# Optimization experiments

Measured on AMD Instinct MI355X. Metric: run time of the kernel, lower is better.

Reference implementation:

```python
import jax, jax.numpy as jnp
import numpy as np

MUL = 128          # multiplicity of each irrep (mul_in == mul_out)
DIMS = (1, 3, 5)   # ir dims for 0e, 1o, 2e
G = 32             # num_indices (weight groups)
N = 2048           # number of elements (rows)
W_FLAT = MUL * MUL * len(DIMS)


def setup_inputs() -> dict:
    key = jax.random.key(0)
    k0, k1, k2, kw = jax.random.split(key, 4)
    x0 = jax.random.normal(k0, (N, MUL, DIMS[0]), jnp.float32)
    x1 = jax.random.normal(k1, (N, MUL, DIMS[1]), jnp.float32)
    x2 = jax.random.normal(k2, (N, MUL, DIMS[2]), jnp.float32)
    w = jax.random.normal(kw, (G, W_FLAT), jnp.float32)
    # variable group sizes summing exactly to N (Repeats(num_index_counts))
    counts = np.random.default_rng(0).multinomial(N, np.ones(G) / G)
    repeats = jnp.asarray(counts, jnp.int32)
    return {"x0": x0, "x1": x1, "x2": x2, "w": w, "repeats": repeats}


def reference(x0, x1, x2, w, repeats):
    # Indexed equivariant linear: row n uses weight group seg[n], where the
    # first repeats[0] rows map to group 0, next repeats[1] rows to group 1, ...
    num_indices = w.shape[0]
    n = x0.shape[0]
    # scale/sqrt(num_indices) from the module times 1/sqrt(mul_in) path norm
    alpha = jnp.float32(1.0 / np.sqrt(num_indices * MUL))
    seg = jnp.searchsorted(jnp.cumsum(repeats), jnp.arange(n), side="right")
    outs = []
    off = 0
    for x in (x0, x1, x2):
        w_ir = w[:, off : off + MUL * MUL].reshape(num_indices, MUL, MUL)
        off += MUL * MUL
        w_el = w_ir[seg]  # (N, mul_in, mul_out) gathered per element
        # x: (N, mul_in, ir_dim) mul_ir layout -> y: (N, mul_out, ir_dim)
        y = jnp.einsum("nmi,nmo->noi", x, w_el) * alpha
        outs.append(y)
    return tuple(outs)
```

## Files before the change

### kernel.cpp

```cpp
#include <hip/hip_runtime.h>


#define NGROUP 32
#define WSTRIDE (128 * 128 * 3)
#define ALPHA 0.015625f

#define CAP0 96
#define CAP01 256
#define GRID_BLOCKS 544

#define LDS_FLOATS 6144

template <int D, int TR, int RP>
__device__ inline void run_ir(int lt, const float* __restrict__ x,
                              const float* __restrict__ w_base_ir,
                              const int* __restrict__ repeats,
                              float* __restrict__ obase,
                              float* __restrict__ Xs) {
  int off = 0, g = -1, row0 = 0, nr = 0;
  int tacc = 0;
  for (int gg = 0; gg < NGROUP; ++gg) {
    int c = repeats[gg];
    int tg = (c + TR - 1) / TR;
    if (lt < tacc + tg) {
      int tig = lt - tacc;
      g = gg;
      row0 = off + tig * TR;
      nr = min(TR, c - tig * TR);
      break;
    }
    tacc += tg;
    off += c;
  }
  if (g < 0) return;

  const int tid = threadIdx.x;
  const int to = tid & 31;
  const int tr = tid >> 5;

  constexpr int ROWELEMS = 128 * D;
  constexpr int BMELEMS = TR * ROWELEMS;

  {
    const float4* xsrc = (const float4*)(x + (size_t)row0 * ROWELEMS);
    float4* xdst = (float4*)Xs;
    const int limit4 = nr * (ROWELEMS / 4);
    constexpr int Q = BMELEMS / 4;
    const float4 z = make_float4(0.f, 0.f, 0.f, 0.f);
    for (int q = tid; q < Q; q += 256) xdst[q] = (q < limit4) ? xsrc[q] : z;
  }
  __syncthreads();

  int xoff[RP];
  int nloc[RP];
  int iofr[RP];
#pragma unroll
  for (int rr = 0; rr < RP; ++rr) {
    int r = tr * RP + rr;
    int nl = r / D;
    int i = r - nl * D;
    nloc[rr] = nl;
    iofr[rr] = i;
    xoff[rr] = nl * ROWELEMS + i;
  }

  const float* w_g = w_base_ir + (size_t)g * WSTRIDE;
  const float4* wp = (const float4*)w_g + to;

  float acc[RP][4];
#pragma unroll
  for (int rr = 0; rr < RP; ++rr)
#pragma unroll
    for (int oj = 0; oj < 4; ++oj) acc[rr][oj] = 0.0f;

#pragma unroll 8
  for (int m = 0; m < 128; ++m) {
    const float4 wf = wp[m * 32];
    float xs[RP];
#pragma unroll
    for (int rr = 0; rr < RP; ++rr) xs[rr] = Xs[xoff[rr] + m * D];
#pragma unroll
    for (int rr = 0; rr < RP; ++rr) {
      acc[rr][0] += xs[rr] * wf.x;
      acc[rr][1] += xs[rr] * wf.y;
      acc[rr][2] += xs[rr] * wf.z;
      acc[rr][3] += xs[rr] * wf.w;
    }
  }

#pragma unroll
  for (int rr = 0; rr < RP; ++rr) {
    if (nloc[rr] < nr) {
      float* orow = obase + (size_t)(row0 + nloc[rr]) * ROWELEMS + iofr[rr];
#pragma unroll
      for (int oj = 0; oj < 4; ++oj)
        orow[(to * 4 + oj) * D] = acc[rr][oj] * ALPHA;
    }
  }
}

__global__ __launch_bounds__(256) void IrrepsIndexedLinear_39161511805249_kernel(
    const float* __restrict__ x0, const float* __restrict__ x1,
    const float* __restrict__ x2, const float* __restrict__ w,
    const int* __restrict__ repeats, float* __restrict__ out) {
  __shared__ float Xs[LDS_FLOATS];

  const int bid = blockIdx.x;
  if (bid < CAP0) {
    run_ir<1, 32, 4>(bid, x0, w, repeats, out, Xs);
  } else if (bid < CAP01) {
    run_ir<3, 16, 6>(bid - CAP0, x1, w + 16384, repeats, out + 262144, Xs);
  } else {
    run_ir<5, 8, 5>(bid - CAP01, x2, w + 32768, repeats, out + 1048576, Xs);
  }
}

extern "C" void kernel_launch(void* const* d_in, const int* in_sizes, int n_in,
                              void* d_out, int out_size, void* d_ws, size_t ws_size,
                              hipStream_t stream) {
  const float* x0 = (const float*)d_in[0];
  const float* x1 = (const float*)d_in[1];
  const float* x2 = (const float*)d_in[2];
  const float* w = (const float*)d_in[3];
  const int* repeats = (const int*)d_in[4];
  float* out = (float*)d_out;

  IrrepsIndexedLinear_39161511805249_kernel<<<GRID_BLOCKS, 256, 0, stream>>>(
      x0, x1, x2, w, repeats, out);
}
```

Before: 93.73 us.

## Use uniform 8-row tiles per irrep with interleaved block mapping and vectorized stores

```diff
diff --git a/kernel.cpp b/kernel.cpp
--- a/kernel.cpp
+++ b/kernel.cpp
@@ -5,29 +5,31 @@
 #define WSTRIDE (128 * 128 * 3)
 #define ALPHA 0.015625f
 
-#define CAP0 96
-#define CAP01 256
-#define GRID_BLOCKS 544
+#define TR 8
+#define PER 27
+#define GRID_BLOCKS 864
+#define LDS_FLOATS 5120
 
-#define LDS_FLOATS 6144
-
-template <int D, int TR, int RP>
+template <int D>
 __device__ inline void run_ir(int lt, const float* __restrict__ x,
                               const float* __restrict__ w_base_ir,
                               const int* __restrict__ repeats,
                               float* __restrict__ obase,
                               float* __restrict__ Xs) {
-  int off = 0, g = -1, row0 = 0, nr = 0;
-  int tacc = 0;
+  int cnt[NGROUP];
+#pragma unroll
+  for (int gg = 0; gg < NGROUP; ++gg) cnt[gg] = repeats[gg];
+
+  int off = 0, g = -1, row0 = 0, nr = 0, tacc = 0;
+#pragma unroll
   for (int gg = 0; gg < NGROUP; ++gg) {
-    int c = repeats[gg];
-    int tg = (c + TR - 1) / TR;
-    if (lt < tacc + tg) {
+    int c = cnt[gg];
+    int tg = (c + TR - 1) >> 3;
+    if (g < 0 && lt < tacc + tg) {
       int tig = lt - tacc;
       g = gg;
       row0 = off + tig * TR;
       nr = min(TR, c - tig * TR);
-      break;
     }
     tacc += tg;
     off += c;
@@ -47,55 +49,48 @@
     const int limit4 = nr * (ROWELEMS / 4);
     constexpr int Q = BMELEMS / 4;
     const float4 z = make_float4(0.f, 0.f, 0.f, 0.f);
+#pragma unroll
     for (int q = tid; q < Q; q += 256) xdst[q] = (q < limit4) ? xsrc[q] : z;
   }
   __syncthreads();
 
-  int xoff[RP];
-  int nloc[RP];
-  int iofr[RP];
-#pragma unroll
-  for (int rr = 0; rr < RP; ++rr) {
-    int r = tr * RP + rr;
-    int nl = r / D;
-    int i = r - nl * D;
-    nloc[rr] = nl;
-    iofr[rr] = i;
-    xoff[rr] = nl * ROWELEMS + i;
-  }
-
   const float* w_g = w_base_ir + (size_t)g * WSTRIDE;
   const float4* wp = (const float4*)w_g + to;
+  const float* xrow = Xs + tr * ROWELEMS;
 
-  float acc[RP][4];
+  float acc[D][4];
 #pragma unroll
-  for (int rr = 0; rr < RP; ++rr)
+  for (int i = 0; i < D; ++i)
 #pragma unroll
-    for (int oj = 0; oj < 4; ++oj) acc[rr][oj] = 0.0f;
+    for (int oj = 0; oj < 4; ++oj) acc[i][oj] = 0.0f;
 
 #pragma unroll 8
   for (int m = 0; m < 128; ++m) {
     const float4 wf = wp[m * 32];
-    float xs[RP];
+    float xs[D];
 #pragma unroll
-    for (int rr = 0; rr < RP; ++rr) xs[rr] = Xs[xoff[rr] + m * D];
+    for (int i = 0; i < D; ++i) xs[i] = xrow[m * D + i];
 #pragma unroll
-    for (int rr = 0; rr < RP; ++rr) {
-      acc[rr][0] += xs[rr] * wf.x;
-      acc[rr][1] += xs[rr] * wf.y;
-      acc[rr][2] += xs[rr] * wf.z;
-      acc[rr][3] += xs[rr] * wf.w;
+    for (int i = 0; i < D; ++i) {
+      acc[i][0] += xs[i] * wf.x;
+      acc[i][1] += xs[i] * wf.y;
+      acc[i][2] += xs[i] * wf.z;
+      acc[i][3] += xs[i] * wf.w;
     }
   }
 
+  if (tr < nr) {
+    float* orow = obase + (size_t)(row0 + tr) * ROWELEMS + to * (4 * D);
+    float vals[4 * D];
 #pragma unroll
-  for (int rr = 0; rr < RP; ++rr) {
-    if (nloc[rr] < nr) {
-      float* orow = obase + (size_t)(row0 + nloc[rr]) * ROWELEMS + iofr[rr];
+    for (int oj = 0; oj < 4; ++oj)
 #pragma unroll
-      for (int oj = 0; oj < 4; ++oj)
-        orow[(to * 4 + oj) * D] = acc[rr][oj] * ALPHA;
-    }
+      for (int i = 0; i < D; ++i) vals[oj * D + i] = acc[i][oj] * ALPHA;
+    float4* o4 = (float4*)orow;
+#pragma unroll
+    for (int q = 0; q < D; ++q)
+      o4[q] = make_float4(vals[4 * q + 0], vals[4 * q + 1], vals[4 * q + 2],
+                          vals[4 * q + 3]);
   }
 }
 
@@ -106,12 +101,14 @@
   __shared__ float Xs[LDS_FLOATS];
 
   const int bid = blockIdx.x;
-  if (bid < CAP0) {
-    run_ir<1, 32, 4>(bid, x0, w, repeats, out, Xs);
-  } else if (bid < CAP01) {
-    run_ir<3, 16, 6>(bid - CAP0, x1, w + 16384, repeats, out + 262144, Xs);
+  const int j = bid / PER;
+  const int k = bid - j * PER;
+  if (k < 9) {
+    run_ir<5>(j * 9 + k, x2, w + 32768, repeats, out + 1048576, Xs);
+  } else if (k < 18) {
+    run_ir<3>(j * 9 + (k - 9), x1, w + 16384, repeats, out + 262144, Xs);
   } else {
-    run_ir<5, 8, 5>(bid - CAP01, x2, w + 32768, repeats, out + 1048576, Xs);
+    run_ir<1>(j * 9 + (k - 18), x0, w, repeats, out, Xs);
   }
 }
 
```

Result: slower. 98.51 us (+5.1%).

## Stage weight chunks through double-buffered LDS with register prefetch

Applied to the files above, without the earlier changes.

```diff
diff --git a/kernel.cpp b/kernel.cpp
--- a/kernel.cpp
+++ b/kernel.cpp
@@ -9,25 +9,31 @@
 #define CAP01 256
 #define GRID_BLOCKS 544
 
-#define LDS_FLOATS 6144
+#define XS_FLOATS 6144
+#define MC 16
+#define NCH 8
+#define WCHUNK (MC * 128)
 
 template <int D, int TR, int RP>
 __device__ inline void run_ir(int lt, const float* __restrict__ x,
                               const float* __restrict__ w_base_ir,
                               const int* __restrict__ repeats,
                               float* __restrict__ obase,
-                              float* __restrict__ Xs) {
-  int off = 0, g = -1, row0 = 0, nr = 0;
-  int tacc = 0;
+                              float* __restrict__ Xs, float* __restrict__ Ws) {
+  int cnt[NGROUP];
+#pragma unroll
+  for (int gg = 0; gg < NGROUP; ++gg) cnt[gg] = repeats[gg];
+
+  int off = 0, g = -1, row0 = 0, nr = 0, tacc = 0;
+#pragma unroll
   for (int gg = 0; gg < NGROUP; ++gg) {
-    int c = repeats[gg];
+    int c = cnt[gg];
     int tg = (c + TR - 1) / TR;
-    if (lt < tacc + tg) {
+    if (g < 0 && lt < tacc + tg) {
       int tig = lt - tacc;
       g = gg;
       row0 = off + tig * TR;
       nr = min(TR, c - tig * TR);
-      break;
     }
     tacc += tg;
     off += c;
@@ -41,13 +47,25 @@
   constexpr int ROWELEMS = 128 * D;
   constexpr int BMELEMS = TR * ROWELEMS;
 
+  const float4* wsrc = (const float4*)(w_base_ir + (size_t)g * WSTRIDE);
+
+  float4 wp0 = wsrc[tid];
+  float4 wp1 = wsrc[256 + tid];
+
   {
     const float4* xsrc = (const float4*)(x + (size_t)row0 * ROWELEMS);
     float4* xdst = (float4*)Xs;
     const int limit4 = nr * (ROWELEMS / 4);
     constexpr int Q = BMELEMS / 4;
     const float4 z = make_float4(0.f, 0.f, 0.f, 0.f);
+#pragma unroll
     for (int q = tid; q < Q; q += 256) xdst[q] = (q < limit4) ? xsrc[q] : z;
+  }
+
+  {
+    float4* wd = (float4*)Ws;
+    wd[tid] = wp0;
+    wd[256 + tid] = wp1;
   }
   __syncthreads();
 
@@ -64,27 +82,42 @@
     xoff[rr] = nl * ROWELEMS + i;
   }
 
-  const float* w_g = w_base_ir + (size_t)g * WSTRIDE;
-  const float4* wp = (const float4*)w_g + to;
-
   float acc[RP][4];
 #pragma unroll
   for (int rr = 0; rr < RP; ++rr)
 #pragma unroll
-    for (int oj = 0; oj < 4; ++oj) acc[rr][oj] = 0.0f;
+    for (int q = 0; q < 4; ++q) acc[rr][q] = 0.0f;
 
-#pragma unroll 8
-  for (int m = 0; m < 128; ++m) {
-    const float4 wf = wp[m * 32];
-    float xs[RP];
+  int cur = 0;
+  for (int c = 0; c < NCH; ++c) {
+    if (c + 1 < NCH) {
+      wp0 = wsrc[(c + 1) * 512 + tid];
+      wp1 = wsrc[(c + 1) * 512 + 256 + tid];
+    }
+    const float* wsh = Ws + cur * WCHUNK + to;
+    const float* xsh = Xs + c * (MC * D);
 #pragma unroll
-    for (int rr = 0; rr < RP; ++rr) xs[rr] = Xs[xoff[rr] + m * D];
+    for (int mm = 0; mm < MC; ++mm) {
+      float wv[4];
 #pragma unroll
-    for (int rr = 0; rr < RP; ++rr) {
-      acc[rr][0] += xs[rr] * wf.x;
-      acc[rr][1] += xs[rr] * wf.y;
-      acc[rr][2] += xs[rr] * wf.z;
-      acc[rr][3] += xs[rr] * wf.w;
+      for (int q = 0; q < 4; ++q) wv[q] = wsh[mm * 128 + 32 * q];
+      float xs[RP];
+#pragma unroll
+      for (int rr = 0; rr < RP; ++rr) xs[rr] = xsh[xoff[rr] + mm * D];
+#pragma unroll
+      for (int rr = 0; rr < RP; ++rr) {
+        acc[rr][0] += xs[rr] * wv[0];
+        acc[rr][1] += xs[rr] * wv[1];
+        acc[rr][2] += xs[rr] * wv[2];
+        acc[rr][3] += xs[rr] * wv[3];
+      }
+    }
+    if (c + 1 < NCH) {
+      float4* wd = (float4*)(Ws + (cur ^ 1) * WCHUNK);
+      wd[tid] = wp0;
+      wd[256 + tid] = wp1;
+      __syncthreads();
+      cur ^= 1;
     }
   }
 
@@ -93,25 +126,26 @@
     if (nloc[rr] < nr) {
       float* orow = obase + (size_t)(row0 + nloc[rr]) * ROWELEMS + iofr[rr];
 #pragma unroll
-      for (int oj = 0; oj < 4; ++oj)
-        orow[(to * 4 + oj) * D] = acc[rr][oj] * ALPHA;
+      for (int q = 0; q < 4; ++q)
+        orow[(to + 32 * q) * D] = acc[rr][q] * ALPHA;
     }
   }
 }
 
-__global__ __launch_bounds__(256) void IrrepsIndexedLinear_39161511805249_kernel(
+__global__ __launch_bounds__(256, 4) void IrrepsIndexedLinear_39161511805249_kernel(
     const float* __restrict__ x0, const float* __restrict__ x1,
     const float* __restrict__ x2, const float* __restrict__ w,
     const int* __restrict__ repeats, float* __restrict__ out) {
-  __shared__ float Xs[LDS_FLOATS];
+  __shared__ float Xs[XS_FLOATS];
+  __shared__ float Ws[2 * WCHUNK];
 
   const int bid = blockIdx.x;
   if (bid < CAP0) {
-    run_ir<1, 32, 4>(bid, x0, w, repeats, out, Xs);
+    run_ir<1, 32, 4>(bid, x0, w, repeats, out, Xs, Ws);
   } else if (bid < CAP01) {
-    run_ir<3, 16, 6>(bid - CAP0, x1, w + 16384, repeats, out + 262144, Xs);
+    run_ir<3, 16, 6>(bid - CAP0, x1, w + 16384, repeats, out + 262144, Xs, Ws);
   } else {
-    run_ir<5, 8, 5>(bid - CAP01, x2, w + 32768, repeats, out + 1048576, Xs);
+    run_ir<5, 8, 5>(bid - CAP01, x2, w + 32768, repeats, out + 1048576, Xs, Ws);
   }
 }
 
```

Result: slower. 104.4 us (+11.4%).

## Reorder block-to-tile mapping, split output columns across wave halves, unroll group search

Applied to the files above, without the earlier changes.

```diff
diff --git a/kernel.cpp b/kernel.cpp
--- a/kernel.cpp
+++ b/kernel.cpp
@@ -5,8 +5,6 @@
 #define WSTRIDE (128 * 128 * 3)
 #define ALPHA 0.015625f
 
-#define CAP0 96
-#define CAP01 256
 #define GRID_BLOCKS 544
 
 #define LDS_FLOATS 6144
@@ -17,17 +15,20 @@
                               const int* __restrict__ repeats,
                               float* __restrict__ obase,
                               float* __restrict__ Xs) {
-  int off = 0, g = -1, row0 = 0, nr = 0;
-  int tacc = 0;
+  int cnt[NGROUP];
+#pragma unroll
+  for (int gg = 0; gg < NGROUP; ++gg) cnt[gg] = repeats[gg];
+
+  int off = 0, g = -1, row0 = 0, nr = 0, tacc = 0;
+#pragma unroll
   for (int gg = 0; gg < NGROUP; ++gg) {
-    int c = repeats[gg];
+    int c = cnt[gg];
     int tg = (c + TR - 1) / TR;
-    if (lt < tacc + tg) {
+    if (g < 0 && lt < tacc + tg) {
       int tig = lt - tacc;
       g = gg;
       row0 = off + tig * TR;
       nr = min(TR, c - tig * TR);
-      break;
     }
     tacc += tg;
     off += c;
@@ -35,8 +36,11 @@
   if (g < 0) return;
 
   const int tid = threadIdx.x;
-  const int to = tid & 31;
-  const int tr = tid >> 5;
+  const int lane = tid & 63;
+  const int wv = tid >> 6;
+  const int h = wv & 1;
+  const int ol = lane & 15;
+  const int slot = ((wv >> 1) << 2) + (lane >> 4);
 
   constexpr int ROWELEMS = 128 * D;
   constexpr int BMELEMS = TR * ROWELEMS;
@@ -47,6 +51,7 @@
     const int limit4 = nr * (ROWELEMS / 4);
     constexpr int Q = BMELEMS / 4;
     const float4 z = make_float4(0.f, 0.f, 0.f, 0.f);
+#pragma unroll
     for (int q = tid; q < Q; q += 256) xdst[q] = (q < limit4) ? xsrc[q] : z;
   }
   __syncthreads();
@@ -56,7 +61,7 @@
   int iofr[RP];
 #pragma unroll
   for (int rr = 0; rr < RP; ++rr) {
-    int r = tr * RP + rr;
+    int r = slot * RP + rr;
     int nl = r / D;
     int i = r - nl * D;
     nloc[rr] = nl;
@@ -65,7 +70,7 @@
   }
 
   const float* w_g = w_base_ir + (size_t)g * WSTRIDE;
-  const float4* wp = (const float4*)w_g + to;
+  const float4* wp = (const float4*)w_g + (h * 16 + ol);
 
   float acc[RP][4];
 #pragma unroll
@@ -88,13 +93,14 @@
     }
   }
 
+  const int ob = h * 64 + ol * 4;
 #pragma unroll
   for (int rr = 0; rr < RP; ++rr) {
     if (nloc[rr] < nr) {
       float* orow = obase + (size_t)(row0 + nloc[rr]) * ROWELEMS + iofr[rr];
 #pragma unroll
       for (int oj = 0; oj < 4; ++oj)
-        orow[(to * 4 + oj) * D] = acc[rr][oj] * ALPHA;
+        orow[(ob + oj) * D] = acc[rr][oj] * ALPHA;
     }
   }
 }
@@ -106,12 +112,20 @@
   __shared__ float Xs[LDS_FLOATS];
 
   const int bid = blockIdx.x;
-  if (bid < CAP0) {
-    run_ir<1, 32, 4>(bid, x0, w, repeats, out, Xs);
-  } else if (bid < CAP01) {
-    run_ir<3, 16, 6>(bid - CAP0, x1, w + 16384, repeats, out + 262144, Xs);
+  const int rank = (bid < 256) ? bid : ((bid < 512) ? (767 - bid) : bid);
+
+  if (rank < 128) {
+    run_ir<3, 16, 6>(rank, x1, w + 16384, repeats, out + 262144, Xs);
+  } else if (rank < 384) {
+    run_ir<5, 8, 5>(rank - 128, x2, w + 32768, repeats, out + 1048576, Xs);
+  } else if (rank < 448) {
+    run_ir<1, 32, 4>(rank - 384, x0, w, repeats, out, Xs);
+  } else if (rank < 480) {
+    run_ir<3, 16, 6>(rank - 320, x1, w + 16384, repeats, out + 262144, Xs);
+  } else if (rank < 512) {
+    run_ir<5, 8, 5>(rank - 224, x2, w + 32768, repeats, out + 1048576, Xs);
   } else {
-    run_ir<5, 8, 5>(bid - CAP01, x2, w + 32768, repeats, out + 1048576, Xs);
+    run_ir<1, 32, 4>(rank - 448, x0, w, repeats, out, Xs);
   }
 }
 
```

Result: slower. 121.6 us (+29.8%).
